# Optimization experiments

Hardware: AMD Instinct MI355X
Metric: run time of the kernel (lower is better)

The kernel has to match this reference:

```python
import jax, jax.numpy as jnp
import numpy as np

H = 32  # hidden_size


def _lstm_scan(x_tbd, Wih, Whh, b):
    # Single-direction LSTM. x_tbd: [T,B,D]; Wih: [4H,D]; Whh: [4H,H]; b: [4H]
    B = x_tbd.shape[1]
    h0 = jnp.zeros((B, Whh.shape[1]), x_tbd.dtype)
    c0 = h0
    xW = jnp.einsum('tbd,gd->tbg', x_tbd, Wih) + b  # precompute input projection [T,B,4H]

    def step(carry, xw):
        h, c = carry
        g = xw + h @ Whh.T
        i, f, gg, o = jnp.split(g, 4, axis=-1)  # PyTorch gate order i,f,g,o
        c = jax.nn.sigmoid(f) * c + jax.nn.sigmoid(i) * jnp.tanh(gg)
        h = jax.nn.sigmoid(o) * jnp.tanh(c)
        return (h, c), h

    _, hs = jax.lax.scan(step, (h0, c0), xW)
    return hs  # [T,B,H]


def _bilstm_layer(x_btd, Wih, Whh, b):
    # x_btd: [B,T,D]; Wih: [2,4H,D] (dir 0 = fwd, 1 = bwd)
    xt = x_btd.transpose(1, 0, 2)
    hf = _lstm_scan(xt, Wih[0], Whh[0], b[0])
    hb = _lstm_scan(xt[::-1], Wih[1], Whh[1], b[1])[::-1]
    return jnp.concatenate([hf, hb], -1).transpose(1, 0, 2)  # [B,T,2H]


def _bilstm(x, Wih0, Whh0, b0, Wih1, Whh1, b1):
    x = _bilstm_layer(x, Wih0, Whh0, b0)
    x = _bilstm_layer(x, Wih1, Whh1, b1)
    return x[:, -1, :]  # [B,2H] (fwd final state | bwd state at last position)


def setup_inputs() -> dict:
    key = jax.random.key(0)
    ks = jax.random.split(key, 20)
    B, T, D = 32768, 30, 4
    k = 1.0 / np.sqrt(H)

    def u(kk, shape):
        return jax.random.uniform(kk, shape, jnp.float32, -k, k)

    inp = {
        'dir_input': jax.random.normal(ks[0], (B, 6), jnp.float32),
        'position_input': jax.random.normal(ks[1], (B, T, D), jnp.float32),
    }
    # lvl and vor bidirectional 2-layer LSTMs; b = b_ih + b_hh combined
    for i, name in enumerate(['lvl', 'vor']):
        o = 2 + i * 6
        inp[name + '_Wih0'] = u(ks[o + 0], (2, 4 * H, D))
        inp[name + '_Whh0'] = u(ks[o + 1], (2, 4 * H, H))
        inp[name + '_b0'] = u(ks[o + 2], (2, 4 * H))
        inp[name + '_Wih1'] = u(ks[o + 3], (2, 4 * H, 2 * H))
        inp[name + '_Whh1'] = u(ks[o + 4], (2, 4 * H, H))
        inp[name + '_b1'] = u(ks[o + 5], (2, 4 * H))
    inp['lvl_fc_W'] = u(ks[14], (2, 2 * H))
    inp['lvl_fc_b'] = u(ks[15], (2,))
    inp['vor_fc_W'] = u(ks[16], (2, 4 * H))
    inp['vor_fc_b'] = u(ks[17], (2,))
    return inp


def reference(dir_input, position_input,
              lvl_Wih0, lvl_Whh0, lvl_b0, lvl_Wih1, lvl_Whh1, lvl_b1,
              vor_Wih0, vor_Whh0, vor_b0, vor_Wih1, vor_Whh1, vor_b1,
              lvl_fc_W, lvl_fc_b, vor_fc_W, vor_fc_b):
    P = 15  # position_len
    dirs = jnp.argmax(dir_input, axis=1)
    dt = position_input.dtype
    mask_vor = ((dirs == 1) | (dirs == 4)).astype(dt)[:, None]
    mask_r = ((dirs == 0) | (dirs == 5)).astype(dt)[:, None]
    mask_l = ((dirs == 2) | (dirs == 3)).astype(dt)[:, None]

    # Batch left/right halves through one LSTM call per branch (same weights)
    halves = jnp.concatenate([position_input[:, :P, :], position_input[:, P:, :]], axis=0)

    lvl_last = _bilstm(halves, lvl_Wih0, lvl_Whh0, lvl_b0, lvl_Wih1, lvl_Whh1, lvl_b1)
    lvl_l, lvl_r = jnp.split(lvl_last, 2, axis=0)
    # dropout is identity in eval mode
    x_r = (lvl_r @ lvl_fc_W.T + lvl_fc_b) * mask_r
    x_l = (lvl_l @ lvl_fc_W.T + lvl_fc_b) * mask_l

    vor_last = _bilstm(halves, vor_Wih0, vor_Whh0, vor_b0, vor_Wih1, vor_Whh1, vor_b1)
    vor_l, vor_r = jnp.split(vor_last, 2, axis=0)
    x_vor = (jnp.concatenate([vor_l, vor_r], axis=1) @ vor_fc_W.T + vor_fc_b) * mask_vor

    return x_r + x_l + x_vor
```

## Files before the change

kernel.cpp:

```cpp
#include <hip/hip_runtime.h>
#include <hip/hip_bf16.h>

typedef _Float16 f16x8 __attribute__((ext_vector_type(8)));
typedef _Float16 f16x4 __attribute__((ext_vector_type(4)));
typedef float    f32x4 __attribute__((ext_vector_type(4)));

#define LOG2E  1.44269504f
#define LOG2E2 2.88539008f

#define HIST_TILE_HALFS 15360
#define LL_OFF_B 62390272
#define LV_OFF_B 62521344
#define CT_OFF_B 62783488

__device__ __forceinline__ float cellT(float fi, float ff, float fg, float fo, float& c) {
    float ei = __builtin_amdgcn_exp2f(fi);
    float ef = __builtin_amdgcn_exp2f(ff);
    float eg = __builtin_amdgcn_exp2f(fg);
    float A  = 1.0f + ef;
    float B  = 1.0f + ei;
    float C  = 1.0f + eg;
    float Cm2 = eg - 1.0f;
    float BC = B * C;
    float cn = fmaf(c, BC, A * Cm2) * __builtin_amdgcn_rcpf(A * BC);
    c = cn;
    float eo = __builtin_amdgcn_exp2f(fo);
    float ec = __builtin_amdgcn_exp2f(LOG2E2 * cn);
    return (ec - 1.0f) * __builtin_amdgcn_rcpf((1.0f + eo) * (1.0f + ec));
}

__device__ __forceinline__ f16x8 afrag8(const float* __restrict__ p, float s) {
    const float4 w0 = *(const float4*)p;
    const float4 w1 = *(const float4*)(p + 4);
    f16x8 v;
    v[0] = (_Float16)(w0.x * s); v[1] = (_Float16)(w0.y * s);
    v[2] = (_Float16)(w0.z * s); v[3] = (_Float16)(w0.w * s);
    v[4] = (_Float16)(w1.x * s); v[5] = (_Float16)(w1.y * s);
    v[6] = (_Float16)(w1.z * s); v[7] = (_Float16)(w1.w * s);
    return v;
}

__device__ __forceinline__ float gscale(int nb) {
    return ((nb >> 1) == 2) ? LOG2E2 : -LOG2E;
}

__device__ __forceinline__ int jperm(int nb, int m) {
    return 8 * (m >> 2) + 4 * (nb & 1) + (m & 3);
}

#define HAVE_K16 __has_builtin(__builtin_amdgcn_mfma_f32_16x16x16f16)

__global__ __launch_bounds__(256) void k0_cls(
    const float* __restrict__ dir_input,
    int* __restrict__ list_lvl, int* __restrict__ list_vor,
    int* __restrict__ cnts)
{
    const int b    = blockIdx.x * 256 + threadIdx.x;
    const int lane = threadIdx.x & 63;

    const float* dp = dir_input + (size_t)b * 6;
    float mx = dp[0];
    int dmax = 0;
#pragma unroll
    for (int i = 1; i < 6; ++i) {
        const float v = dp[i];
        if (v > mx) { mx = v; dmax = i; }
    }
    const bool isv = (dmax == 1) || (dmax == 4);
    const int  hf  = (dmax == 0 || dmax == 5) ? 1 : 0;

    {
        const unsigned long long mk = __ballot(!isv);
        const int n = __popcll(mk);
        if (n) {
            const int leader = __ffsll((unsigned long long)mk) - 1;
            int base = 0;
            if (lane == leader) base = atomicAdd(&cnts[0], n);
            base = __shfl(base, leader);
            if (!isv) {
                const int rank = __popcll(mk & ((1ull << lane) - 1ull));
                list_lvl[base + rank] = b | (hf << 15);
            }
        }
    }
    {
        const unsigned long long mv = __ballot(isv);
        const int n = __popcll(mv);
        if (n) {
            const int leader = __ffsll((unsigned long long)mv) - 1;
            int base = 0;
            if (lane == leader) base = atomicAdd(&cnts[1], 2 * n);
            base = __shfl(base, leader);
            if (isv) {
                const int rank = __popcll(mv & ((1ull << lane) - 1ull));
                list_vor[base + 2 * rank]     = b;
                list_vor[base + 2 * rank + 1] = b | (1 << 15);
            }
        }
    }
}

__global__ __launch_bounds__(256, 4) void k1_l0(
    const float* __restrict__ pos,
    const float* __restrict__ lvl_Wih0, const float* __restrict__ lvl_Whh0,
    const float* __restrict__ lvl_b0,
    const float* __restrict__ vor_Wih0, const float* __restrict__ vor_Whh0,
    const float* __restrict__ vor_b0,
    _Float16* __restrict__ hist,
    const int* __restrict__ list_lvl, const int* __restrict__ list_vor,
    const int* __restrict__ cnts)
{
    const int lane = threadIdx.x & 63;
    const int wv   = threadIdx.x >> 6;
    const int n0   = lane & 15;
    const int quad = lane >> 4;
    const int tile = blockIdx.x * 4 + wv;
    const int m    = blockIdx.y >> 1;
    const int dir  = blockIdx.y & 1;

    const int cnt = cnts[m];
    if (tile * 16 >= cnt) return;

    const int* list = m ? list_vor : list_lvl;
    const int  li   = tile * 16 + n0;
    const int  e    = (li < cnt) ? list[li] : 0;
    const int  b    = e & 32767;
    const int  hf   = (e >> 15) & 1;

    const float* Wih = (m ? vor_Wih0 : lvl_Wih0) + dir * 128 * 4;
    const float* Whh = (m ? vor_Whh0 : lvl_Whh0) + dir * 128 * 32;
    const float* bs  = (m ? vor_b0   : lvl_b0)   + dir * 128;

    f16x8 WhhA[8];
#if HAVE_K16
    f16x4 WihA[8];
#else
    f16x8 WihA[8];
#endif
#pragma unroll
    for (int nb = 0; nb < 8; ++nb) {
        const int J = (nb >> 1) * 32 + jperm(nb, n0);
        const float s = gscale(nb);
        WhhA[nb] = afrag8(Whh + J * 32 + quad * 8, s);
#if HAVE_K16
        f16x4 v = {(_Float16)0.0f, (_Float16)0.0f, (_Float16)0.0f, (_Float16)0.0f};
        if (quad == 0) {
            const float4 w = *(const float4*)(Wih + J * 4);
            v[0] = (_Float16)(w.x * s); v[1] = (_Float16)(w.y * s);
            v[2] = (_Float16)(w.z * s); v[3] = (_Float16)(w.w * s);
        } else if (quad == 1) {
            v[0] = (_Float16)(bs[J] * s);
        }
        WihA[nb] = v;
#else
        f16x8 v;
#pragma unroll
        for (int r = 0; r < 8; ++r) v[r] = (_Float16)0.0f;
        if (quad == 0) {
            const float4 w = *(const float4*)(Wih + J * 4);
            v[0] = (_Float16)(w.x * s); v[1] = (_Float16)(w.y * s);
            v[2] = (_Float16)(w.z * s); v[3] = (_Float16)(w.w * s);
            v[4] = (_Float16)(bs[J] * s);
        }
        WihA[nb] = v;
#endif
    }

    const float* xp = pos + ((size_t)b * 30 + hf * 15 + (dir ? 14 : 0)) * 4;
    const int xstep = dir ? -4 : 4;

    _Float16* hp = hist + ((size_t)(m * 2048 + tile)) * HIST_TILE_HALFS
                 + (size_t)(dir ? 14 : 0) * 1024 + dir * 512 + lane * 8;
    const int hstep = dir ? -1024 : 1024;

    float c[4][2];
#pragma unroll
    for (int r = 0; r < 4; ++r) { c[r][0] = 0.0f; c[r][1] = 0.0f; }

    f16x8 hB;
#pragma unroll
    for (int r = 0; r < 8; ++r) hB[r] = (_Float16)0.0f;

    const f32x4 z4 = {0.0f, 0.0f, 0.0f, 0.0f};

    float4 xn = *(const float4*)xp;

#pragma unroll 1
    for (int ti = 0; ti < 15; ++ti) {
        const float4 xv = xn;
        const int tn = (ti < 14) ? (ti + 1) : ti;
        xn = *(const float4*)(xp + tn * xstep);

#if HAVE_K16
        f16x4 xB = {(_Float16)0.0f, (_Float16)0.0f, (_Float16)0.0f, (_Float16)0.0f};
        if (quad == 0) {
            xB[0] = (_Float16)xv.x; xB[1] = (_Float16)xv.y;
            xB[2] = (_Float16)xv.z; xB[3] = (_Float16)xv.w;
        } else if (quad == 1) {
            xB[0] = (_Float16)1.0f;
        }
#else
        f16x8 xB;
#pragma unroll
        for (int r = 0; r < 8; ++r) xB[r] = (_Float16)0.0f;
        if (quad == 0) {
            xB[0] = (_Float16)xv.x; xB[1] = (_Float16)xv.y;
            xB[2] = (_Float16)xv.z; xB[3] = (_Float16)xv.w;
            xB[4] = (_Float16)1.0f;
        }
#endif

        f32x4 acc[8];
#pragma unroll
        for (int nb = 0; nb < 8; ++nb)
#if HAVE_K16
            acc[nb] = __builtin_amdgcn_mfma_f32_16x16x16f16(WihA[nb], xB, z4, 0, 0, 0);
#else
            acc[nb] = __builtin_amdgcn_mfma_f32_16x16x32_f16(WihA[nb], xB, z4, 0, 0, 0);
#endif
#pragma unroll
        for (int nb = 0; nb < 8; ++nb)
            acc[nb] = __builtin_amdgcn_mfma_f32_16x16x32_f16(WhhA[nb], hB, acc[nb], 0, 0, 0);

        f16x8 nh;
#pragma unroll
        for (int r = 0; r < 4; ++r) {
            nh[r]     = (_Float16)cellT(acc[0][r], acc[2][r], acc[4][r], acc[6][r], c[r][0]);
            nh[4 + r] = (_Float16)cellT(acc[1][r], acc[3][r], acc[5][r], acc[7][r], c[r][1]);
        }
        hB = nh;

        *(f16x8*)hp = hB;
        hp += hstep;
    }
}

__global__ __launch_bounds__(256, 2) void k2_l1(
    const float* __restrict__ lvl_Wih1, const float* __restrict__ lvl_Whh1,
    const float* __restrict__ lvl_b1,
    const float* __restrict__ vor_Wih1, const float* __restrict__ vor_Whh1,
    const float* __restrict__ vor_b1,
    const float* __restrict__ lvl_fc_W, const float* __restrict__ lvl_fc_b,
    const float* __restrict__ vor_fc_W, const float* __restrict__ vor_fc_b,
    const _Float16* __restrict__ hist, float* __restrict__ out,
    const int* __restrict__ list_lvl, const int* __restrict__ list_vor,
    const int* __restrict__ cnts)
{
    const int lane  = threadIdx.x & 63;
    const int wv    = threadIdx.x >> 6;
    const int n0    = lane & 15;
    const int quad  = lane >> 4;
    const int tpair = (blockIdx.x * 4 + wv) * 2;
    const int m     = blockIdx.y;

    const int cnt = cnts[m];
    if (tpair * 16 >= cnt) return;

    const int* list = m ? list_vor : list_lvl;

    const float* Wih = m ? vor_Wih1 : lvl_Wih1;
    const float* Whh = m ? vor_Whh1 : lvl_Whh1;
    const float* bs  = m ? vor_b1   : lvl_b1;

    f16x8 WA[8], WB[8], WH[8];
    f32x4 biasv[8];
#pragma unroll
    for (int nb = 0; nb < 8; ++nb) {
        const int g = nb >> 1, p = nb & 1;
        const int J = g * 32 + jperm(nb, n0);
        const float s = gscale(nb);
        WA[nb] = afrag8(Wih + J * 64 + quad * 8, s);
        WB[nb] = afrag8(Wih + J * 64 + 32 + quad * 8, s);
        WH[nb] = afrag8(Whh + J * 32 + quad * 8, s);
        const float4 bq = *(const float4*)(bs + g * 32 + 8 * quad + 4 * p);
        f32x4 bv; bv[0] = bq.x * s; bv[1] = bq.y * s; bv[2] = bq.z * s; bv[3] = bq.w * s;
        biasv[nb] = bv;
    }

    const _Float16* hb[2];
#pragma unroll
    for (int tt = 0; tt < 2; ++tt)
        hb[tt] = hist + ((size_t)(m * 2048 + tpair + tt)) * HIST_TILE_HALFS + lane * 8;

    float c1[2][4][2];
#pragma unroll
    for (int tt = 0; tt < 2; ++tt)
#pragma unroll
        for (int r = 0; r < 4; ++r) { c1[tt][r][0] = 0.0f; c1[tt][r][1] = 0.0f; }
    f16x8 h1B[2];
#pragma unroll
    for (int tt = 0; tt < 2; ++tt)
#pragma unroll
        for (int r = 0; r < 8; ++r) h1B[tt][r] = (_Float16)0.0f;
    float h1f_a[2][4], h1f_b[2][4];
    f16x8 a_f[2], a_b[2];

    f16x8 nf[2], nb2[2];
#pragma unroll
    for (int tt = 0; tt < 2; ++tt) {
        nf[tt]  = *(const f16x8*)(hb[tt]);
        nb2[tt] = *(const f16x8*)(hb[tt] + 512);
    }

#pragma unroll 1
    for (int t = 0; t < 15; ++t) {
#pragma unroll
        for (int tt = 0; tt < 2; ++tt) { a_f[tt] = nf[tt]; a_b[tt] = nb2[tt]; }
        const int tn = (t < 14) ? (t + 1) : t;
#pragma unroll
        for (int tt = 0; tt < 2; ++tt) {
            nf[tt]  = *(const f16x8*)(hb[tt] + (size_t)tn * 1024);
            nb2[tt] = *(const f16x8*)(hb[tt] + (size_t)tn * 1024 + 512);
        }

#pragma unroll
        for (int tt = 0; tt < 2; ++tt) {
            f32x4 acc[8];
#pragma unroll
            for (int nb = 0; nb < 8; ++nb)
                acc[nb] = __builtin_amdgcn_mfma_f32_16x16x32_f16(WA[nb], a_f[tt], biasv[nb], 0, 0, 0);
#pragma unroll
            for (int nb = 0; nb < 8; ++nb)
                acc[nb] = __builtin_amdgcn_mfma_f32_16x16x32_f16(WB[nb], a_b[tt], acc[nb], 0, 0, 0);
#pragma unroll
            for (int nb = 0; nb < 8; ++nb)
                acc[nb] = __builtin_amdgcn_mfma_f32_16x16x32_f16(WH[nb], h1B[tt], acc[nb], 0, 0, 0);

            f16x8 nh;
#pragma unroll
            for (int r = 0; r < 4; ++r) {
                float ha  = cellT(acc[0][r], acc[2][r], acc[4][r], acc[6][r], c1[tt][r][0]);
                float hbv = cellT(acc[1][r], acc[3][r], acc[5][r], acc[7][r], c1[tt][r][1]);
                h1f_a[tt][r] = ha; h1f_b[tt][r] = hbv;
                nh[r] = (_Float16)ha; nh[4 + r] = (_Float16)hbv;
            }
            h1B[tt] = nh;
        }
    }

    float h1b_a[2][4], h1b_b[2][4];
    {
        const float* Wb = Wih + 128 * 64;
        const float* bb = bs + 128;
        const int nbs[6] = {0, 1, 4, 5, 6, 7};
        f32x4 accb[2][6];
#pragma unroll
        for (int q6 = 0; q6 < 6; ++q6) {
            const int nb = nbs[q6];
            const int g = nb >> 1, p = nb & 1;
            const int J = g * 32 + jperm(nb, n0);
            const float s = gscale(nb);
            const f16x8 wa = afrag8(Wb + J * 64 + quad * 8, s);
            const f16x8 wb = afrag8(Wb + J * 64 + 32 + quad * 8, s);
            const float4 bq = *(const float4*)(bb + g * 32 + 8 * quad + 4 * p);
            f32x4 bv; bv[0] = bq.x * s; bv[1] = bq.y * s; bv[2] = bq.z * s; bv[3] = bq.w * s;
#pragma unroll
            for (int tt = 0; tt < 2; ++tt) {
                f32x4 a = __builtin_amdgcn_mfma_f32_16x16x32_f16(wa, a_f[tt], bv, 0, 0, 0);
                a = __builtin_amdgcn_mfma_f32_16x16x32_f16(wb, a_b[tt], a, 0, 0, 0);
                accb[tt][q6] = a;
            }
        }
#pragma unroll
        for (int tt = 0; tt < 2; ++tt)
#pragma unroll
            for (int r = 0; r < 4; ++r) {
#pragma unroll
                for (int p = 0; p < 2; ++p) {
                    const float i_ = accb[tt][0 + p][r];
                    const float g_ = accb[tt][2 + p][r];
                    const float o_ = accb[tt][4 + p][r];
                    float ei = __builtin_amdgcn_exp2f(i_);
                    float eg = __builtin_amdgcn_exp2f(g_);
                    float Bv = 1.0f + ei;
                    float C  = 1.0f + eg;
                    float cv = (eg - 1.0f) * __builtin_amdgcn_rcpf(Bv * C);
                    float eo = __builtin_amdgcn_exp2f(o_);
                    float ec = __builtin_amdgcn_exp2f(LOG2E2 * cv);
                    float h = (ec - 1.0f) * __builtin_amdgcn_rcpf((1.0f + eo) * (1.0f + ec));
                    if (p == 0) h1b_a[tt][r] = h; else h1b_b[tt][r] = h;
                }
            }
    }

#pragma unroll
    for (int tt = 0; tt < 2; ++tt) {
        const int  li    = (tpair + tt) * 16 + n0;
        const bool valid = li < cnt;
        const int  e     = valid ? list[li] : 0;
        const int  b     = e & 32767;
        const int  hf    = (e >> 15) & 1;

        float pr[2];
#pragma unroll
        for (int o = 0; o < 2; ++o) {
            const float* Wr = (m == 0) ? (lvl_fc_W + o * 64)
                                       : (vor_fc_W + o * 128 + hf * 64);
            const float4 wfa = *(const float4*)(Wr + 8 * quad);
            const float4 wfb = *(const float4*)(Wr + 8 * quad + 4);
            const float4 wba = *(const float4*)(Wr + 32 + 8 * quad);
            const float4 wbb = *(const float4*)(Wr + 32 + 8 * quad + 4);
            float a = wfa.x * h1f_a[tt][0] + wfa.y * h1f_a[tt][1]
                    + wfa.z * h1f_a[tt][2] + wfa.w * h1f_a[tt][3];
            a += wfb.x * h1f_b[tt][0] + wfb.y * h1f_b[tt][1]
               + wfb.z * h1f_b[tt][2] + wfb.w * h1f_b[tt][3];
            a += wba.x * h1b_a[tt][0] + wba.y * h1b_a[tt][1]
               + wba.z * h1b_a[tt][2] + wba.w * h1b_a[tt][3];
            a += wbb.x * h1b_b[tt][0] + wbb.y * h1b_b[tt][1]
               + wbb.z * h1b_b[tt][2] + wbb.w * h1b_b[tt][3];
            pr[o] = a;
        }
#pragma unroll
        for (int o = 0; o < 2; ++o) {
            pr[o] += __shfl_xor(pr[o], 16);
            pr[o] += __shfl_xor(pr[o], 32);
        }

        if (quad == 0 && valid) {
            float b0v, b1v;
            if (m == 0) { b0v = lvl_fc_b[0]; b1v = lvl_fc_b[1]; }
            else        { b0v = hf ? 0.0f : vor_fc_b[0]; b1v = hf ? 0.0f : vor_fc_b[1]; }
            atomicAdd(out + (size_t)b * 2 + 0, pr[0] + b0v);
            atomicAdd(out + (size_t)b * 2 + 1, pr[1] + b1v);
        }
    }
}

extern "C" void kernel_launch(void* const* d_in, const int* in_sizes, int n_in,
                              void* d_out, int out_size, void* d_ws, size_t ws_size,
                              hipStream_t stream) {
    const float* dir_input = (const float*)d_in[0];
    const float* pos       = (const float*)d_in[1];
    const float* lvl_Wih0  = (const float*)d_in[2];
    const float* lvl_Whh0  = (const float*)d_in[3];
    const float* lvl_b0    = (const float*)d_in[4];
    const float* lvl_Wih1  = (const float*)d_in[5];
    const float* lvl_Whh1  = (const float*)d_in[6];
    const float* lvl_b1    = (const float*)d_in[7];
    const float* vor_Wih0  = (const float*)d_in[8];
    const float* vor_Whh0  = (const float*)d_in[9];
    const float* vor_b0    = (const float*)d_in[10];
    const float* vor_Wih1  = (const float*)d_in[11];
    const float* vor_Whh1  = (const float*)d_in[12];
    const float* vor_b1    = (const float*)d_in[13];
    const float* lvl_fc_W  = (const float*)d_in[14];
    const float* lvl_fc_b  = (const float*)d_in[15];
    const float* vor_fc_W  = (const float*)d_in[16];
    const float* vor_fc_b  = (const float*)d_in[17];
    float* out = (float*)d_out;
    _Float16* hist = (_Float16*)d_ws;
    char* wsb = (char*)d_ws;

    int* list_lvl = (int*)(wsb + LL_OFF_B);
    int* list_vor = (int*)(wsb + LV_OFF_B);
    int* cnts     = (int*)(wsb + CT_OFF_B);

    (void)in_sizes; (void)n_in; (void)ws_size;

    hipMemsetAsync(d_out, 0, (size_t)out_size * sizeof(float), stream);
    hipMemsetAsync(cnts, 0, 2 * sizeof(int), stream);

    dim3 blk(256, 1, 1);
    hipLaunchKernelGGL(k0_cls, dim3(128, 1, 1), blk, 0, stream,
                       dir_input, list_lvl, list_vor, cnts);

    hipLaunchKernelGGL(k1_l0, dim3(512, 4, 1), blk, 0, stream,
                       pos, lvl_Wih0, lvl_Whh0, lvl_b0,
                       vor_Wih0, vor_Whh0, vor_b0,
                       hist, list_lvl, list_vor, cnts);

    hipLaunchKernelGGL(k2_l1, dim3(256, 2, 1), blk, 0, stream,
                       lvl_Wih1, lvl_Whh1, lvl_b1,
                       vor_Wih1, vor_Whh1, vor_b1,
                       lvl_fc_W, lvl_fc_b, vor_fc_W, vor_fc_b,
                       hist, out, list_lvl, list_vor, cnts);
}
```

Baseline: 223.8 us.

## Move recurrent weights and biases to LDS and prefetch history two steps ahead

The layer-1 kernel now keeps the Whh fragments and scaled biases in shared memory and reloads them inside the time loop, instead of holding them in registers for the whole kernel. This cuts register pressure. The history loads are now double-buffered two timesteps ahead, which gives memory latency more time to hide. The costs are extra LDS reads per step, a __syncthreads during setup, and more registers spent on the deeper prefetch.

```diff
diff --git a/kernel.cpp b/kernel.cpp
--- a/kernel.cpp
+++ b/kernel.cpp
@@ -253,29 +253,42 @@
     const int tpair = (blockIdx.x * 4 + wv) * 2;
     const int m     = blockIdx.y;
 
-    const int cnt = cnts[m];
-    if (tpair * 16 >= cnt) return;
-
-    const int* list = m ? list_vor : list_lvl;
-
     const float* Wih = m ? vor_Wih1 : lvl_Wih1;
     const float* Whh = m ? vor_Whh1 : lvl_Whh1;
     const float* bs  = m ? vor_b1   : lvl_b1;
 
-    f16x8 WA[8], WB[8], WH[8];
-    f32x4 biasv[8];
-#pragma unroll
-    for (int nb = 0; nb < 8; ++nb) {
-        const int g = nb >> 1, p = nb & 1;
-        const int J = g * 32 + jperm(nb, n0);
-        const float s = gscale(nb);
-        WA[nb] = afrag8(Wih + J * 64 + quad * 8, s);
-        WB[nb] = afrag8(Wih + J * 64 + 32 + quad * 8, s);
-        WH[nb] = afrag8(Whh + J * 32 + quad * 8, s);
-        const float4 bq = *(const float4*)(bs + g * 32 + 8 * quad + 4 * p);
-        f32x4 bv; bv[0] = bq.x * s; bv[1] = bq.y * s; bv[2] = bq.z * s; bv[3] = bq.w * s;
-        biasv[nb] = bv;
-    }
+    __shared__ __align__(16) _Float16 whlds[8 * 64 * 8];
+    __shared__ __align__(16) float    blds[8 * 64 * 4];
+
+    if (threadIdx.x < 64) {
+#pragma unroll
+        for (int nb = 0; nb < 8; ++nb) {
+            const int g = nb >> 1, p = nb & 1;
+            const int J = g * 32 + jperm(nb, n0);
+            const float s = gscale(nb);
+            *(f16x8*)(whlds + ((size_t)nb * 64 + lane) * 8) = afrag8(Whh + J * 32 + quad * 8, s);
+            const float4 bq = *(const float4*)(bs + g * 32 + 8 * quad + 4 * p);
+            f32x4 bv; bv[0] = bq.x * s; bv[1] = bq.y * s; bv[2] = bq.z * s; bv[3] = bq.w * s;
+            *(f32x4*)(blds + ((size_t)nb * 64 + lane) * 4) = bv;
+        }
+    }
+
+    const int cnt = cnts[m];
+    const bool active = (tpair * 16 < cnt);
+    const int* list = m ? list_vor : list_lvl;
+
+    f16x8 WA[8], WB[8];
+    if (active) {
+#pragma unroll
+        for (int nb = 0; nb < 8; ++nb) {
+            const int J = (nb >> 1) * 32 + jperm(nb, n0);
+            const float s = gscale(nb);
+            WA[nb] = afrag8(Wih + J * 64 + quad * 8, s);
+            WB[nb] = afrag8(Wih + J * 64 + 32 + quad * 8, s);
+        }
+    }
+    __syncthreads();
+    if (!active) return;
 
     const _Float16* hb[2];
 #pragma unroll
@@ -295,36 +308,45 @@
     float h1f_a[2][4], h1f_b[2][4];
     f16x8 a_f[2], a_b[2];
 
-    f16x8 nf[2], nb2[2];
+    f16x8 nf0[2], nb0[2], nf1[2], nb1[2];
 #pragma unroll
     for (int tt = 0; tt < 2; ++tt) {
-        nf[tt]  = *(const f16x8*)(hb[tt]);
-        nb2[tt] = *(const f16x8*)(hb[tt] + 512);
+        nf0[tt] = *(const f16x8*)(hb[tt]);
+        nb0[tt] = *(const f16x8*)(hb[tt] + 512);
+        nf1[tt] = *(const f16x8*)(hb[tt] + 1024);
+        nb1[tt] = *(const f16x8*)(hb[tt] + 1024 + 512);
     }
 
 #pragma unroll 1
     for (int t = 0; t < 15; ++t) {
 #pragma unroll
-        for (int tt = 0; tt < 2; ++tt) { a_f[tt] = nf[tt]; a_b[tt] = nb2[tt]; }
-        const int tn = (t < 14) ? (t + 1) : t;
-#pragma unroll
         for (int tt = 0; tt < 2; ++tt) {
-            nf[tt]  = *(const f16x8*)(hb[tt] + (size_t)tn * 1024);
-            nb2[tt] = *(const f16x8*)(hb[tt] + (size_t)tn * 1024 + 512);
+            a_f[tt] = nf0[tt]; a_b[tt] = nb0[tt];
+            nf0[tt] = nf1[tt]; nb0[tt] = nb1[tt];
+        }
+        const int tn2 = (t < 13) ? (t + 2) : 14;
+#pragma unroll
+        for (int tt = 0; tt < 2; ++tt) {
+            nf1[tt] = *(const f16x8*)(hb[tt] + (size_t)tn2 * 1024);
+            nb1[tt] = *(const f16x8*)(hb[tt] + (size_t)tn2 * 1024 + 512);
         }
 
 #pragma unroll
         for (int tt = 0; tt < 2; ++tt) {
             f32x4 acc[8];
 #pragma unroll
-            for (int nb = 0; nb < 8; ++nb)
-                acc[nb] = __builtin_amdgcn_mfma_f32_16x16x32_f16(WA[nb], a_f[tt], biasv[nb], 0, 0, 0);
+            for (int nb = 0; nb < 8; ++nb) {
+                const f32x4 bv = *(const f32x4*)(blds + ((size_t)nb * 64 + lane) * 4);
+                acc[nb] = __builtin_amdgcn_mfma_f32_16x16x32_f16(WA[nb], a_f[tt], bv, 0, 0, 0);
+            }
 #pragma unroll
             for (int nb = 0; nb < 8; ++nb)
                 acc[nb] = __builtin_amdgcn_mfma_f32_16x16x32_f16(WB[nb], a_b[tt], acc[nb], 0, 0, 0);
 #pragma unroll
-            for (int nb = 0; nb < 8; ++nb)
-                acc[nb] = __builtin_amdgcn_mfma_f32_16x16x32_f16(WH[nb], h1B[tt], acc[nb], 0, 0, 0);
+            for (int nb = 0; nb < 8; ++nb) {
+                const f16x8 wh = *(const f16x8*)(whlds + ((size_t)nb * 64 + lane) * 8);
+                acc[nb] = __builtin_amdgcn_mfma_f32_16x16x32_f16(wh, h1B[tt], acc[nb], 0, 0, 0);
+            }
 
             f16x8 nh;
 #pragma unroll
```

New measurement: 221.7 us. No clear change (-0.9%).
